# Performance work log

Hardware: AMD Instinct MI355X
Metric: run time of the kernel (lower is better)

Reference implementation:

```python
import jax, jax.numpy as jnp
import numpy as np

B, T, C, H = 2, 2048, 1024, 16
D = C // H  # head dim = 64
EPS = 1e-5


def setup_inputs() -> dict:
    key = jax.random.key(0)
    k1, k2, k3 = jax.random.split(key, 3)
    x = jax.random.normal(k1, (B, T, C), dtype=jnp.float32)
    W_attn = jax.random.normal(k2, (3 * C, C), dtype=jnp.float32) * 0.02
    W_proj = jax.random.normal(k3, (C, C), dtype=jnp.float32) * 0.02
    # standard RoPE inverse frequencies, one per rotation pair (D//2)
    rope_freqs = 1.0 / (10000.0 ** (jnp.arange(D // 2, dtype=jnp.float32) * 2.0 / D))
    ln_weight = jnp.ones((C,), dtype=jnp.float32)
    ln_bias = jnp.zeros((C,), dtype=jnp.float32)
    return {"x": x, "rope_freqs": rope_freqs, "W_attn": W_attn,
            "W_proj": W_proj, "ln_weight": ln_weight, "ln_bias": ln_bias}


def _apply_rope(q, k, freqs):
    # q,k: [B,H,S,D]; matches torch apply_rope: split even/odd, concat halves
    S = q.shape[-2]
    theta = jnp.arange(S, dtype=q.dtype)[:, None] * freqs[None, :]  # [S, D/2]
    sin_t, cos_t = jnp.sin(theta), jnp.cos(theta)

    def rot(t):
        t1, t2 = t[..., 0::2], t[..., 1::2]
        return jnp.concatenate([t1 * cos_t - t2 * sin_t,
                                t1 * sin_t + t2 * cos_t], axis=-1)

    return rot(q), rot(k)


def reference(x, rope_freqs, W_attn, W_proj, ln_weight, ln_bias):
    Bv, Tv, Cv = x.shape
    qkv = x @ W_attn.T                      # [B,T,3C] (F.linear, no bias)
    q, k, v = jnp.split(qkv, 3, axis=-1)
    resh = lambda t: t.reshape(Bv, Tv, H, D).transpose(0, 2, 1, 3)  # [B,H,T,D]
    q, k, v = resh(q), resh(k), resh(v)
    q, k = _apply_rope(q, k, rope_freqs)
    scale = 1.0 / jnp.sqrt(jnp.asarray(D, dtype=x.dtype))
    scores = jnp.einsum('bhqd,bhkd->bhqk', q, k) * scale
    causal = jnp.tril(jnp.ones((Tv, Tv), dtype=bool))
    scores = jnp.where(causal[None, None], scores, -jnp.inf)
    att = jax.nn.softmax(scores, axis=-1)
    y = jnp.einsum('bhqk,bhkd->bhqd', att, v)
    y = y.transpose(0, 2, 1, 3).reshape(Bv, Tv, Cv)
    y = y @ W_proj.T                        # c_proj (bias=False)
    # resid dropout is identity in eval; LayerNorm (eps=1e-5, biased var)
    mean = jnp.mean(y, axis=-1, keepdims=True)
    var = jnp.mean(jnp.square(y - mean), axis=-1, keepdims=True)
    return (y - mean) / jnp.sqrt(var + EPS) * ln_weight + ln_bias
```

## Files before the change

kernel.cpp:

```cpp
#include <hip/hip_runtime.h>
#include <hip/hip_bf16.h>
#include <math.h>

typedef short bf16x8 __attribute__((ext_vector_type(8)));
typedef float f32x4 __attribute__((ext_vector_type(4)));

#define T_SEQ 2048
#define C_DIM 1024
#define H_HEADS 16
#define D_HEAD 64
#define BT 4096
#define C3 3072
#define BH 32

static __device__ inline unsigned short bf_bits(float f) {
    __hip_bfloat16 h = __float2bfloat16(f);
    unsigned short u;
    __builtin_memcpy(&u, &h, 2);
    return u;
}

static __device__ inline unsigned int cvtpk(float lo, float hi) {
    unsigned int r;
    asm("v_cvt_pk_bf16_f32 %0, %1, %2" : "=v"(r) : "v"(lo), "v"(hi));
    return r;
}

__device__ __forceinline__ void gload16(const void* g, void* l) {
    __builtin_amdgcn_global_load_lds(
        (const __attribute__((address_space(1))) void*)g,
        (__attribute__((address_space(3))) void*)l, 16, 0, 0);
}

__device__ __forceinline__ int swz(int r) {
    return ((((r & 3) ^ ((r >> 3) & 3)) | (((r >> 3) & 1) << 2)) << 3);
}

__global__ void prep_kernel(const float* __restrict__ x,
                            const float* __restrict__ Wa,
                            const float* __restrict__ Wp,
                            const float* __restrict__ freqs,
                            __hip_bfloat16* __restrict__ xb,
                            __hip_bfloat16* __restrict__ Wab,
                            __hip_bfloat16* __restrict__ Wpb,
                            float2* __restrict__ tab) {
    const int bidx = blockIdx.x, tid = threadIdx.x;
    if (bidx < 8192) {
        const float* src;
        __hip_bfloat16* dst;
        int i;
        if (bidx < 4096)      { src = x;  dst = xb;  i = bidx * 256 + tid; }
        else if (bidx < 7168) { src = Wa; dst = Wab; i = (bidx - 4096) * 256 + tid; }
        else                  { src = Wp; dst = Wpb; i = (bidx - 7168) * 256 + tid; }
        float4 v = reinterpret_cast<const float4*>(src)[i];
        ushort4 o;
        o.x = bf_bits(v.x); o.y = bf_bits(v.y); o.z = bf_bits(v.z); o.w = bf_bits(v.w);
        reinterpret_cast<ushort4*>(dst)[i] = o;
    } else {
        int idx = (bidx - 8192) * 256 + tid;
        int i = idx & 31, tp = idx >> 5;
        float th = (float)tp * freqs[i];
        tab[idx] = make_float2(cosf(th), sinf(th));
    }
}

template<int MODE, int BN>
__global__ __launch_bounds__(256) void gemm_bt(
    const __hip_bfloat16* __restrict__ A,
    const __hip_bfloat16* __restrict__ Bw,
    void* __restrict__ Cout, int M, int N, int K,
    const float2* __restrict__ tab,
    __hip_bfloat16* __restrict__ q_s,
    __hip_bfloat16* __restrict__ k_s,
    __hip_bfloat16* __restrict__ v_t) {
    __shared__ __hip_bfloat16 As[128][64];
    __shared__ __hip_bfloat16 Bs[BN][64];
    const int t = threadIdx.x;
    const int lane = t & 63, w = t >> 6;
    const int wr = w >> 1, wc = w & 1;
    const int l15 = lane & 15, lg = lane >> 4;
    const int m0 = blockIdx.y * 128, n0 = blockIdx.x * BN;

    const int srow = lane >> 3;
    const int scol = ((lane & 7) ^ srow) * 8;
    const int xr = (l15 & 7) << 3;

    constexpr int NF = BN / 32;
    f32x4 acc[4][NF];
    f32x4 zero4 = {0.f, 0.f, 0.f, 0.f};
#pragma unroll
    for (int m = 0; m < 4; m++)
#pragma unroll
        for (int n = 0; n < NF; n++) acc[m][n] = zero4;

    const int nt = K >> 6;
    for (int tk = 0; tk < nt; tk++) {
        const int k0 = tk << 6;
#pragma unroll
        for (int i = 0; i < 4; i++) {
            int rbase = w * 32 + i * 8;
            gload16(&A[(size_t)(m0 + rbase + srow) * K + k0 + scol], &As[rbase][0]);
        }
#pragma unroll
        for (int i = 0; i < NF; i++) {
            int rbase = w * (BN / 4) + i * 8;
            gload16(&Bw[(size_t)(n0 + rbase + srow) * K + k0 + scol], &Bs[rbase][0]);
        }
        __syncthreads();
#pragma unroll
        for (int kk = 0; kk < 2; kk++) {
            bf16x8 a[4], b[NF];
            const int co = (kk * 32 + lg * 8) ^ xr;
#pragma unroll
            for (int m = 0; m < 4; m++)
                a[m] = *reinterpret_cast<const bf16x8*>(&As[wr * 64 + m * 16 + l15][co]);
#pragma unroll
            for (int n = 0; n < NF; n++)
                b[n] = *reinterpret_cast<const bf16x8*>(&Bs[wc * (BN / 2) + n * 16 + l15][co]);
            __builtin_amdgcn_s_setprio(1);
#pragma unroll
            for (int m = 0; m < 4; m++)
#pragma unroll
                for (int n = 0; n < NF; n++)
                    acc[m][n] = __builtin_amdgcn_mfma_f32_16x16x32_bf16(a[m], b[n], acc[m][n], 0, 0, 0);
            __builtin_amdgcn_s_setprio(0);
        }
        __syncthreads();
    }

    if (MODE == 2) {
        const int region = n0 >> 10;
#pragma unroll
        for (int m = 0; m < 4; m++)
#pragma unroll
            for (int n = 0; n < NF; n++) {
                const int col = n0 + wc * (BN / 2) + n * 16 + l15;
                const int d = col & 63;
                const int h = (col >> 6) & 15;
                const int row0 = m0 + wr * 64 + m * 16 + lg * 4;
                const int b = row0 >> 11;
                const int tp0 = row0 & 2047;
                if (region < 2) {
                    const int i = d >> 1, odd = d & 1;
                    const int dp = (d >> 1) + (odd ? 32 : 0);
                    __hip_bfloat16* dst = (region == 0) ? q_s : k_s;
                    const float sc = (region == 0) ? 0.125f * 1.44269504f : 1.0f;
#pragma unroll
                    for (int jj = 0; jj < 4; jj++) {
                        float own = acc[m][n][jj];
                        float par = __shfl_xor(own, 1);
                        float2 cs = tab[(tp0 + jj) * 32 + i];
                        float val = own * cs.x + (odd ? par : -par) * cs.y;
                        dst[((size_t)(b * H_HEADS + h) * T_SEQ + tp0 + jj) * D_HEAD + dp] =
                            __float2bfloat16(val * sc);
                    }
                } else {
                    ushort4 ov;
                    ov.x = bf_bits(acc[m][n][0]);
                    ov.y = bf_bits(acc[m][n][1]);
                    ov.z = bf_bits(acc[m][n][2]);
                    ov.w = bf_bits(acc[m][n][3]);
                    *reinterpret_cast<ushort4*>(
                        &v_t[((size_t)(b * H_HEADS + h) * D_HEAD + d) * T_SEQ + tp0]) = ov;
                }
            }
        return;
    }

#pragma unroll
    for (int m = 0; m < 4; m++)
#pragma unroll
        for (int n = 0; n < NF; n++)
#pragma unroll
            for (int jj = 0; jj < 4; jj++) {
                int row = m0 + wr * 64 + m * 16 + lg * 4 + jj;
                int col = n0 + wc * (BN / 2) + n * 16 + l15;
                ((__hip_bfloat16*)Cout)[(size_t)row * N + col] = __float2bfloat16(acc[m][n][jj]);
            }
}

__global__ __launch_bounds__(256, 4) void attn_kernel(
    const __hip_bfloat16* __restrict__ q_s,
    const __hip_bfloat16* __restrict__ k_s,
    const __hip_bfloat16* __restrict__ v_t,
    __hip_bfloat16* __restrict__ y) {
    __shared__ ushort Kbuf[2][64 * 64];
    __shared__ ushort Vbuf[2][64 * 64];

    const int bid = blockIdx.x;
    const int qt = 31 - (bid >> 5);
    const int bh = bid & 31;
    const int t = threadIdx.x, lane = t & 63, w = t >> 6;
    const int l15 = lane & 15, lg = lane >> 4;
    const size_t hbase = (size_t)bh * T_SEQ * D_HEAD;
    const int qr = qt * 64 + w * 16 + l15;

    bf16x8 aq[2];
#pragma unroll
    for (int dd = 0; dd < 2; dd++)
        aq[dd] = *reinterpret_cast<const bf16x8*>(&q_s[hbase + (size_t)qr * 64 + dd * 32 + lg * 8]);

    bf16x8 ones;
#pragma unroll
    for (int i = 0; i < 8; i++) ones[i] = (short)0x3F80;

    f32x4 zero4 = {0.f, 0.f, 0.f, 0.f};
    f32x4 o[4];
#pragma unroll
    for (int dc = 0; dc < 4; dc++) o[dc] = zero4;
    f32x4 lacc = zero4;
    float mr = -INFINITY;

    int koff[4][2], voff[4][2];
#pragma unroll
    for (int c = 0; c < 4; c++) {
        int kro = ((c >> 1) << 5) + ((c & 1) << 2) + ((l15 >> 2) << 3) + (l15 & 3);
        int sz = swz(kro);
#pragma unroll
        for (int dd = 0; dd < 2; dd++)
            koff[c][dd] = kro * 64 + ((dd * 32 + lg * 8) ^ sz);
    }
#pragma unroll
    for (int dc = 0; dc < 4; dc++) {
        int vro = dc * 16 + l15;
        int sz = swz(vro);
#pragma unroll
        for (int dd = 0; dd < 2; dd++)
            voff[dc][dd] = vro * 64 + ((dd * 32 + lg * 8) ^ sz);
    }

    const int srow = t >> 3;
    const int sgr = t & 7;

    auto stageKV = [&](int buf, int kbase) {
#pragma unroll
        for (int i = 0; i < 2; i++) {
            int r = i * 32 + srow;
            int gsw = (sgr ^ (swz(r) >> 3)) * 8;
            gload16(&k_s[hbase + (size_t)(kbase + r) * 64 + gsw],
                    &Kbuf[buf][(i * 32 + w * 8) * 64]);
            gload16(&v_t[hbase + (size_t)r * T_SEQ + kbase + gsw],
                    &Vbuf[buf][(i * 32 + w * 8) * 64]);
        }
    };

    int cur = 0;
    stageKV(0, 0);
    __syncthreads();

    for (int kt = 0; kt <= qt; kt++) {
        const int kt64 = kt << 6;
        if (kt < qt) stageKV(cur ^ 1, kt64 + 64);

        const ushort* Kc = Kbuf[cur];
        const ushort* Vc = Vbuf[cur];
        bf16x8 kf[4][2], av[4][2];
#pragma unroll
        for (int c = 0; c < 4; c++)
#pragma unroll
            for (int dd = 0; dd < 2; dd++)
                kf[c][dd] = *reinterpret_cast<const bf16x8*>(&Kc[koff[c][dd]]);
#pragma unroll
        for (int dc = 0; dc < 4; dc++)
#pragma unroll
            for (int dd = 0; dd < 2; dd++)
                av[dc][dd] = *reinterpret_cast<const bf16x8*>(&Vc[voff[dc][dd]]);

        f32x4 st[4];
        __builtin_amdgcn_s_setprio(1);
#pragma unroll
        for (int c = 0; c < 4; c++) {
            st[c] = zero4;
#pragma unroll
            for (int dd = 0; dd < 2; dd++)
                st[c] = __builtin_amdgcn_mfma_f32_16x16x32_bf16(kf[c][dd], aq[dd], st[c], 0, 0, 0);
        }
        __builtin_amdgcn_s_setprio(0);

        if (kt == qt) {
#pragma unroll
            for (int c = 0; c < 4; c++) {
                int kb = kt64 + ((c >> 1) << 5) + ((c & 1) << 2) + lg * 8;
#pragma unroll
                for (int jj = 0; jj < 4; jj++)
                    if (kb + jj > qr) st[c][jj] = -INFINITY;
            }
        }

        float m0a = fmaxf(st[0][0], st[0][1]), m0b = fmaxf(st[0][2], st[0][3]);
        float m1a = fmaxf(st[1][0], st[1][1]), m1b = fmaxf(st[1][2], st[1][3]);
        float m2a = fmaxf(st[2][0], st[2][1]), m2b = fmaxf(st[2][2], st[2][3]);
        float m3a = fmaxf(st[3][0], st[3][1]), m3b = fmaxf(st[3][2], st[3][3]);
        float lmx = fmaxf(fmaxf(fmaxf(m0a, m0b), fmaxf(m1a, m1b)),
                          fmaxf(fmaxf(m2a, m2b), fmaxf(m3a, m3b)));

        if (__any(lmx - mr > 8.f)) {
            float mx = fmaxf(lmx, __shfl_xor(lmx, 16));
            mx = fmaxf(mx, __shfl_xor(mx, 32));
            float mnew = fmaxf(mr, mx);
            float scl = __builtin_amdgcn_exp2f(mr - mnew);
            mr = mnew;
            lacc[0] *= scl;
#pragma unroll
            for (int dc = 0; dc < 4; dc++)
#pragma unroll
                for (int jj = 0; jj < 4; jj++) o[dc][jj] *= scl;
        }

#pragma unroll
        for (int c = 0; c < 4; c++)
#pragma unroll
            for (int jj = 0; jj < 4; jj++)
                st[c][jj] = __builtin_amdgcn_exp2f(st[c][jj] - mr);

        union { bf16x8 v; unsigned int u[4]; } pf0, pf1;
        pf0.u[0] = cvtpk(st[0][0], st[0][1]);
        pf0.u[1] = cvtpk(st[0][2], st[0][3]);
        pf0.u[2] = cvtpk(st[1][0], st[1][1]);
        pf0.u[3] = cvtpk(st[1][2], st[1][3]);
        pf1.u[0] = cvtpk(st[2][0], st[2][1]);
        pf1.u[1] = cvtpk(st[2][2], st[2][3]);
        pf1.u[2] = cvtpk(st[3][0], st[3][1]);
        pf1.u[3] = cvtpk(st[3][2], st[3][3]);

        __builtin_amdgcn_s_setprio(1);
        lacc = __builtin_amdgcn_mfma_f32_16x16x32_bf16(ones, pf0.v, lacc, 0, 0, 0);
        lacc = __builtin_amdgcn_mfma_f32_16x16x32_bf16(ones, pf1.v, lacc, 0, 0, 0);
#pragma unroll
        for (int dc = 0; dc < 4; dc++) {
            o[dc] = __builtin_amdgcn_mfma_f32_16x16x32_bf16(av[dc][0], pf0.v, o[dc], 0, 0, 0);
            o[dc] = __builtin_amdgcn_mfma_f32_16x16x32_bf16(av[dc][1], pf1.v, o[dc], 0, 0, 0);
        }
        __builtin_amdgcn_s_setprio(0);

        __syncthreads();
        cur ^= 1;
    }

    const int b = bh >> 4, h = bh & 15;
    float inv = 1.f / lacc[0];
#pragma unroll
    for (int dc = 0; dc < 4; dc++) {
        ushort4 ov;
        ov.x = bf_bits(o[dc][0] * inv);
        ov.y = bf_bits(o[dc][1] * inv);
        ov.z = bf_bits(o[dc][2] * inv);
        ov.w = bf_bits(o[dc][3] * inv);
        *reinterpret_cast<ushort4*>(
            &y[(size_t)(b * T_SEQ + qr) * C_DIM + h * 64 + dc * 16 + lg * 4]) = ov;
    }
}

__global__ __launch_bounds__(256) void ln_kernel(const __hip_bfloat16* __restrict__ y2,
                                                 const float* __restrict__ wgt,
                                                 const float* __restrict__ bias,
                                                 float* __restrict__ out) {
    const int row = blockIdx.x;
    const int t = threadIdx.x;
    ushort4 u = reinterpret_cast<const ushort4*>(y2 + (size_t)row * C_DIM)[t];
    float4 v;
    v.x = __bfloat162float(*(__hip_bfloat16*)&u.x);
    v.y = __bfloat162float(*(__hip_bfloat16*)&u.y);
    v.z = __bfloat162float(*(__hip_bfloat16*)&u.z);
    v.w = __bfloat162float(*(__hip_bfloat16*)&u.w);
    float s = v.x + v.y + v.z + v.w;
    float s2 = v.x * v.x + v.y * v.y + v.z * v.z + v.w * v.w;
#pragma unroll
    for (int d = 1; d < 64; d <<= 1) {
        s += __shfl_xor(s, d);
        s2 += __shfl_xor(s2, d);
    }
    __shared__ float ps[4], ps2[4];
    const int lane = t & 63, w = t >> 6;
    if (lane == 0) { ps[w] = s; ps2[w] = s2; }
    __syncthreads();
    s = ps[0] + ps[1] + ps[2] + ps[3];
    s2 = ps2[0] + ps2[1] + ps2[2] + ps2[3];
    float mean = s * (1.f / C_DIM);
    float var = s2 * (1.f / C_DIM) - mean * mean;
    float inv = rsqrtf(var + 1e-5f);
    float4 wv = reinterpret_cast<const float4*>(wgt)[t];
    float4 bv = reinterpret_cast<const float4*>(bias)[t];
    float4 ov;
    ov.x = (v.x - mean) * inv * wv.x + bv.x;
    ov.y = (v.y - mean) * inv * wv.y + bv.y;
    ov.z = (v.z - mean) * inv * wv.z + bv.z;
    ov.w = (v.w - mean) * inv * wv.w + bv.w;
    reinterpret_cast<float4*>(out + (size_t)row * C_DIM)[t] = ov;
}

extern "C" void kernel_launch(void* const* d_in, const int* in_sizes, int n_in,
                              void* d_out, int out_size, void* d_ws, size_t ws_size,
                              hipStream_t stream) {
    const float* x      = (const float*)d_in[0];
    const float* freqs  = (const float*)d_in[1];
    const float* W_attn = (const float*)d_in[2];
    const float* W_proj = (const float*)d_in[3];
    const float* lnw    = (const float*)d_in[4];
    const float* lnb    = (const float*)d_in[5];
    float* out = (float*)d_out;
    char* ws = (char*)d_ws;

    __hip_bfloat16* xb   = (__hip_bfloat16*)(ws);
    __hip_bfloat16* Wab  = (__hip_bfloat16*)(ws + 8388608);
    __hip_bfloat16* Wpb  = (__hip_bfloat16*)(ws + 14680064);
    float2*         tab  = (float2*)(ws + 16777216);
    __hip_bfloat16* q_s  = (__hip_bfloat16*)(ws + 41943040);
    __hip_bfloat16* k_s  = (__hip_bfloat16*)(ws + 50331648);
    __hip_bfloat16* v_t  = (__hip_bfloat16*)(ws + 58720256);
    __hip_bfloat16* y_at = (__hip_bfloat16*)(ws + 67108864);
    __hip_bfloat16* y2b  = (__hip_bfloat16*)(ws + 75497472);

    prep_kernel<<<8448, 256, 0, stream>>>(x, W_attn, W_proj, freqs, xb, Wab, Wpb, tab);

    gemm_bt<2, 128><<<dim3(C3 / 128, BT / 128), 256, 0, stream>>>(
        xb, Wab, nullptr, BT, C3, C_DIM, tab, q_s, k_s, v_t);

    attn_kernel<<<1024, 256, 0, stream>>>(q_s, k_s, v_t, y_at);

    gemm_bt<1, 64><<<dim3(C_DIM / 64, BT / 128), 256, 0, stream>>>(
        y_at, Wpb, y2b, BT, C_DIM, C_DIM, nullptr, nullptr, nullptr, nullptr);

    ln_kernel<<<BT, 256, 0, stream>>>(y2b, lnw, lnb, out);
}
```

Before: 104.2 us.

## Process two 64-row query tiles per attention block to reuse staged K/V

Each attention block now covers 128 query rows: two per-wave 16-row fragments with separate online-softmax state. Every staged 64-key K/V tile feeds both fragments, which halves K/V global loads and LDS staging per query row, and the grid is halved to 512 blocks. In exchange each thread holds roughly twice the registers, so launch bounds drop to 2 blocks per CU. Fewer, longer blocks with uneven causal work may also worsen load balance across CUs.

```diff
diff --git a/kernel.cpp b/kernel.cpp
--- a/kernel.cpp
+++ b/kernel.cpp
@@ -179,7 +179,7 @@
             }
 }
 
-__global__ __launch_bounds__(256, 4) void attn_kernel(
+__global__ __launch_bounds__(256, 2) void attn_kernel(
     const __hip_bfloat16* __restrict__ q_s,
     const __hip_bfloat16* __restrict__ k_s,
     const __hip_bfloat16* __restrict__ v_t,
@@ -188,28 +188,32 @@
     __shared__ ushort Vbuf[2][64 * 64];
 
     const int bid = blockIdx.x;
-    const int qt = 31 - (bid >> 5);
+    const int qt = 15 - (bid >> 5);
     const int bh = bid & 31;
     const int t = threadIdx.x, lane = t & 63, w = t >> 6;
     const int l15 = lane & 15, lg = lane >> 4;
     const size_t hbase = (size_t)bh * T_SEQ * D_HEAD;
-    const int qr = qt * 64 + w * 16 + l15;
-
-    bf16x8 aq[2];
-#pragma unroll
-    for (int dd = 0; dd < 2; dd++)
-        aq[dd] = *reinterpret_cast<const bf16x8*>(&q_s[hbase + (size_t)qr * 64 + dd * 32 + lg * 8]);
+    const int qb = qt * 128;
+    const int fb0 = qb + w * 16, fb1 = qb + 64 + w * 16;
+    const int qr0 = fb0 + l15, qr1 = fb1 + l15;
+
+    bf16x8 aq0[2], aq1[2];
+#pragma unroll
+    for (int dd = 0; dd < 2; dd++) {
+        aq0[dd] = *reinterpret_cast<const bf16x8*>(&q_s[hbase + (size_t)qr0 * 64 + dd * 32 + lg * 8]);
+        aq1[dd] = *reinterpret_cast<const bf16x8*>(&q_s[hbase + (size_t)qr1 * 64 + dd * 32 + lg * 8]);
+    }
 
     bf16x8 ones;
 #pragma unroll
     for (int i = 0; i < 8; i++) ones[i] = (short)0x3F80;
 
     f32x4 zero4 = {0.f, 0.f, 0.f, 0.f};
-    f32x4 o[4];
-#pragma unroll
-    for (int dc = 0; dc < 4; dc++) o[dc] = zero4;
-    f32x4 lacc = zero4;
-    float mr = -INFINITY;
+    f32x4 o0[4], o1[4];
+#pragma unroll
+    for (int dc = 0; dc < 4; dc++) { o0[dc] = zero4; o1[dc] = zero4; }
+    f32x4 lacc0 = zero4, lacc1 = zero4;
+    float mr0 = -INFINITY, mr1 = -INFINITY;
 
     int koff[4][2], voff[4][2];
 #pragma unroll
@@ -248,9 +252,10 @@
     stageKV(0, 0);
     __syncthreads();
 
-    for (int kt = 0; kt <= qt; kt++) {
+    const int last = 2 * qt + 1;
+    for (int kt = 0; kt <= last; kt++) {
         const int kt64 = kt << 6;
-        if (kt < qt) stageKV(cur ^ 1, kt64 + 64);
+        if (kt < last) stageKV(cur ^ 1, kt64 + 64);
 
         const ushort* Kc = Kbuf[cur];
         const ushort* Vc = Vbuf[cur];
@@ -266,88 +271,102 @@
             for (int dd = 0; dd < 2; dd++)
                 av[dc][dd] = *reinterpret_cast<const bf16x8*>(&Vc[voff[dc][dd]]);
 
-        f32x4 st[4];
-        __builtin_amdgcn_s_setprio(1);
-#pragma unroll
-        for (int c = 0; c < 4; c++) {
-            st[c] = zero4;
-#pragma unroll
-            for (int dd = 0; dd < 2; dd++)
-                st[c] = __builtin_amdgcn_mfma_f32_16x16x32_bf16(kf[c][dd], aq[dd], st[c], 0, 0, 0);
-        }
-        __builtin_amdgcn_s_setprio(0);
-
-        if (kt == qt) {
+        auto frag_step = [&](const bf16x8 (&aq)[2], f32x4 (&o)[4], f32x4& lacc,
+                             float& mr, int fb, int qr) {
+            f32x4 st[4];
+            __builtin_amdgcn_s_setprio(1);
 #pragma unroll
             for (int c = 0; c < 4; c++) {
-                int kb = kt64 + ((c >> 1) << 5) + ((c & 1) << 2) + lg * 8;
+                st[c] = zero4;
+#pragma unroll
+                for (int dd = 0; dd < 2; dd++)
+                    st[c] = __builtin_amdgcn_mfma_f32_16x16x32_bf16(kf[c][dd], aq[dd], st[c], 0, 0, 0);
+            }
+            __builtin_amdgcn_s_setprio(0);
+
+            if (kt64 + 63 > fb) {
+#pragma unroll
+                for (int c = 0; c < 4; c++) {
+                    int kb = kt64 + ((c >> 1) << 5) + ((c & 1) << 2) + lg * 8;
+#pragma unroll
+                    for (int jj = 0; jj < 4; jj++)
+                        if (kb + jj > qr) st[c][jj] = -INFINITY;
+                }
+            }
+
+            float m0a = fmaxf(st[0][0], st[0][1]), m0b = fmaxf(st[0][2], st[0][3]);
+            float m1a = fmaxf(st[1][0], st[1][1]), m1b = fmaxf(st[1][2], st[1][3]);
+            float m2a = fmaxf(st[2][0], st[2][1]), m2b = fmaxf(st[2][2], st[2][3]);
+            float m3a = fmaxf(st[3][0], st[3][1]), m3b = fmaxf(st[3][2], st[3][3]);
+            float lmx = fmaxf(fmaxf(fmaxf(m0a, m0b), fmaxf(m1a, m1b)),
+                              fmaxf(fmaxf(m2a, m2b), fmaxf(m3a, m3b)));
+
+            if (__any(lmx - mr > 8.f)) {
+                float mx = fmaxf(lmx, __shfl_xor(lmx, 16));
+                mx = fmaxf(mx, __shfl_xor(mx, 32));
+                float mnew = fmaxf(mr, mx);
+                float scl = __builtin_amdgcn_exp2f(mr - mnew);
+                mr = mnew;
+                lacc[0] *= scl;
+#pragma unroll
+                for (int dc = 0; dc < 4; dc++)
+#pragma unroll
+                    for (int jj = 0; jj < 4; jj++) o[dc][jj] *= scl;
+            }
+
+#pragma unroll
+            for (int c = 0; c < 4; c++)
 #pragma unroll
                 for (int jj = 0; jj < 4; jj++)
-                    if (kb + jj > qr) st[c][jj] = -INFINITY;
-            }
-        }
-
-        float m0a = fmaxf(st[0][0], st[0][1]), m0b = fmaxf(st[0][2], st[0][3]);
-        float m1a = fmaxf(st[1][0], st[1][1]), m1b = fmaxf(st[1][2], st[1][3]);
-        float m2a = fmaxf(st[2][0], st[2][1]), m2b = fmaxf(st[2][2], st[2][3]);
-        float m3a = fmaxf(st[3][0], st[3][1]), m3b = fmaxf(st[3][2], st[3][3]);
-        float lmx = fmaxf(fmaxf(fmaxf(m0a, m0b), fmaxf(m1a, m1b)),
-                          fmaxf(fmaxf(m2a, m2b), fmaxf(m3a, m3b)));
-
-        if (__any(lmx - mr > 8.f)) {
-            float mx = fmaxf(lmx, __shfl_xor(lmx, 16));
-            mx = fmaxf(mx, __shfl_xor(mx, 32));
-            float mnew = fmaxf(mr, mx);
-            float scl = __builtin_amdgcn_exp2f(mr - mnew);
-            mr = mnew;
-            lacc[0] *= scl;
-#pragma unroll
-            for (int dc = 0; dc < 4; dc++)
-#pragma unroll
-                for (int jj = 0; jj < 4; jj++) o[dc][jj] *= scl;
-        }
-
-#pragma unroll
-        for (int c = 0; c < 4; c++)
-#pragma unroll
-            for (int jj = 0; jj < 4; jj++)
-                st[c][jj] = __builtin_amdgcn_exp2f(st[c][jj] - mr);
-
-        union { bf16x8 v; unsigned int u[4]; } pf0, pf1;
-        pf0.u[0] = cvtpk(st[0][0], st[0][1]);
-        pf0.u[1] = cvtpk(st[0][2], st[0][3]);
-        pf0.u[2] = cvtpk(st[1][0], st[1][1]);
-        pf0.u[3] = cvtpk(st[1][2], st[1][3]);
-        pf1.u[0] = cvtpk(st[2][0], st[2][1]);
-        pf1.u[1] = cvtpk(st[2][2], st[2][3]);
-        pf1.u[2] = cvtpk(st[3][0], st[3][1]);
-        pf1.u[3] = cvtpk(st[3][2], st[3][3]);
-
-        __builtin_amdgcn_s_setprio(1);
-        lacc = __builtin_amdgcn_mfma_f32_16x16x32_bf16(ones, pf0.v, lacc, 0, 0, 0);
-        lacc = __builtin_amdgcn_mfma_f32_16x16x32_bf16(ones, pf1.v, lacc, 0, 0, 0);
-#pragma unroll
-        for (int dc = 0; dc < 4; dc++) {
-            o[dc] = __builtin_amdgcn_mfma_f32_16x16x32_bf16(av[dc][0], pf0.v, o[dc], 0, 0, 0);
-            o[dc] = __builtin_amdgcn_mfma_f32_16x16x32_bf16(av[dc][1], pf1.v, o[dc], 0, 0, 0);
-        }
-        __builtin_amdgcn_s_setprio(0);
+                    st[c][jj] = __builtin_amdgcn_exp2f(st[c][jj] - mr);
+
+            union { bf16x8 v; unsigned int u[4]; } pf0, pf1;
+            pf0.u[0] = cvtpk(st[0][0], st[0][1]);
+            pf0.u[1] = cvtpk(st[0][2], st[0][3]);
+            pf0.u[2] = cvtpk(st[1][0], st[1][1]);
+            pf0.u[3] = cvtpk(st[1][2], st[1][3]);
+            pf1.u[0] = cvtpk(st[2][0], st[2][1]);
+            pf1.u[1] = cvtpk(st[2][2], st[2][3]);
+            pf1.u[2] = cvtpk(st[3][0], st[3][1]);
+            pf1.u[3] = cvtpk(st[3][2], st[3][3]);
+
+            __builtin_amdgcn_s_setprio(1);
+            lacc = __builtin_amdgcn_mfma_f32_16x16x32_bf16(ones, pf0.v, lacc, 0, 0, 0);
+            lacc = __builtin_amdgcn_mfma_f32_16x16x32_bf16(ones, pf1.v, lacc, 0, 0, 0);
+#pragma unroll
+            for (int dc = 0; dc < 4; dc++) {
+                o[dc] = __builtin_amdgcn_mfma_f32_16x16x32_bf16(av[dc][0], pf0.v, o[dc], 0, 0, 0);
+                o[dc] = __builtin_amdgcn_mfma_f32_16x16x32_bf16(av[dc][1], pf1.v, o[dc], 0, 0, 0);
+            }
+            __builtin_amdgcn_s_setprio(0);
+        };
+
+        frag_step(aq1, o1, lacc1, mr1, fb1, qr1);
+        if (kt64 <= fb0 + 15)
+            frag_step(aq0, o0, lacc0, mr0, fb0, qr0);
 
         __syncthreads();
         cur ^= 1;
     }
 
     const int b = bh >> 4, h = bh & 15;
-    float inv = 1.f / lacc[0];
+    float inv0 = 1.f / lacc0[0], inv1 = 1.f / lacc1[0];
 #pragma unroll
     for (int dc = 0; dc < 4; dc++) {
         ushort4 ov;
-        ov.x = bf_bits(o[dc][0] * inv);
-        ov.y = bf_bits(o[dc][1] * inv);
-        ov.z = bf_bits(o[dc][2] * inv);
-        ov.w = bf_bits(o[dc][3] * inv);
+        ov.x = bf_bits(o0[dc][0] * inv0);
+        ov.y = bf_bits(o0[dc][1] * inv0);
+        ov.z = bf_bits(o0[dc][2] * inv0);
+        ov.w = bf_bits(o0[dc][3] * inv0);
         *reinterpret_cast<ushort4*>(
-            &y[(size_t)(b * T_SEQ + qr) * C_DIM + h * 64 + dc * 16 + lg * 4]) = ov;
+            &y[(size_t)(b * T_SEQ + qr0) * C_DIM + h * 64 + dc * 16 + lg * 4]) = ov;
+        ushort4 o2;
+        o2.x = bf_bits(o1[dc][0] * inv1);
+        o2.y = bf_bits(o1[dc][1] * inv1);
+        o2.z = bf_bits(o1[dc][2] * inv1);
+        o2.w = bf_bits(o1[dc][3] * inv1);
+        *reinterpret_cast<ushort4*>(
+            &y[(size_t)(b * T_SEQ + qr1) * C_DIM + h * 64 + dc * 16 + lg * 4]) = o2;
     }
 }
 
@@ -416,7 +435,7 @@
     gemm_bt<2, 128><<<dim3(C3 / 128, BT / 128), 256, 0, stream>>>(
         xb, Wab, nullptr, BT, C3, C_DIM, tab, q_s, k_s, v_t);
 
-    attn_kernel<<<1024, 256, 0, stream>>>(q_s, k_s, v_t, y_at);
+    attn_kernel<<<512, 256, 0, stream>>>(q_s, k_s, v_t, y_at);
 
     gemm_bt<1, 64><<<dim3(C_DIM / 64, BT / 128), 256, 0, stream>>>(
         y_at, Wpb, y2b, BT, C_DIM, C_DIM, nullptr, nullptr, nullptr, nullptr);
```

Result: slower. 115.4 us (+10.8%).
